# Optimization experiments

Hardware: AMD Instinct MI355X
Metric: run time of the kernel (lower is better)

## Reference

```python
import jax, jax.numpy as jnp
import numpy as np

NEG_SLOPE = 0.2   # PyG GATConv default negative_slope
NUM_GRAPHS = 64   # graphs per batched timestep (max batch id + 1)


def setup_inputs() -> dict:
    key = jax.random.key(0)
    ks = jax.random.split(key, 16)
    T, N, E, F, H, C, B = 8, 20000, 320000, 128, 128, 16, NUM_GRAPHS
    x = jax.random.normal(ks[0], (T, N, F), dtype=jnp.float32)
    edge_index = jax.random.randint(ks[1], (T, 2, E), 0, N, dtype=jnp.int32)
    batch = jnp.sort(jax.random.randint(ks[2], (N,), 0, B, dtype=jnp.int32))
    z = jax.random.normal(ks[3], (B, H), dtype=jnp.float32)
    s_f = 1.0 / np.sqrt(F)
    s_h = 1.0 / np.sqrt(H)
    return {
        "x": x, "edge_index": edge_index, "batch": batch, "z": z,
        "gat_W": jax.random.normal(ks[4], (F, H), jnp.float32) * s_f,
        "att_src": jax.random.normal(ks[5], (H,), jnp.float32) * s_h,
        "att_dst": jax.random.normal(ks[6], (H,), jnp.float32) * s_h,
        "gat_bias": jnp.zeros((H,), jnp.float32),
        "W_ih": jax.random.normal(ks[7], (4 * H, H), jnp.float32) * s_h,
        "W_hh": jax.random.normal(ks[8], (4 * H, H), jnp.float32) * s_h,
        "b_ih": jnp.zeros((4 * H,), jnp.float32),
        "b_hh": jnp.zeros((4 * H,), jnp.float32),
        "fc_W": jax.random.normal(ks[9], (C, 2 * H), jnp.float32) * (1.0 / np.sqrt(2 * H)),
        "fc_b": jnp.zeros((C,), jnp.float32),
    }


def _gat_conv(x, edge_index, W, a_src, a_dst, bias):
    # PyG GATConv, heads=1, add_self_loops=True: gather -> softmax-per-target -> scatter
    N = x.shape[0]
    h = x @ W                                        # [N, H]
    loops = jnp.arange(N, dtype=edge_index.dtype)
    src = jnp.concatenate([edge_index[0], loops])    # message source j
    dst = jnp.concatenate([edge_index[1], loops])    # message target i
    e = jax.nn.leaky_relu((h @ a_src)[src] + (h @ a_dst)[dst], NEG_SLOPE)  # [E+N]
    m = jax.ops.segment_max(e, dst, num_segments=N)  # stable softmax over incoming edges
    w = jnp.exp(e - m[dst])
    denom = jax.ops.segment_sum(w, dst, num_segments=N)
    alpha = w / denom[dst]
    out = jax.ops.segment_sum(alpha[:, None] * h[src], dst, num_segments=N)
    return out + bias


def reference(x, edge_index, batch, z, gat_W, att_src, att_dst, gat_bias,
              W_ih, W_hh, b_ih, b_hh, fc_W, fc_b):
    B = NUM_GRAPHS
    # per-timestep GAT (vmapped over the window) + global mean pool
    node_feats = jax.vmap(lambda xt, ei: _gat_conv(xt, ei, gat_W, att_src, att_dst, gat_bias))(x, edge_index)  # [T,N,H]
    counts = jnp.maximum(jax.ops.segment_sum(jnp.ones_like(batch, jnp.float32), batch, num_segments=B), 1.0)
    pooled = jax.vmap(lambda f: jax.ops.segment_sum(f, batch, num_segments=B))(node_feats) / counts[None, :, None]  # [T,B,H]

    # LSTM over T (PyTorch gate order i, f, g, o)
    H = gat_W.shape[1]
    h0 = jnp.zeros((B, H), x.dtype)

    def step(carry, xt):
        h, c = carry
        gates = xt @ W_ih.T + b_ih + h @ W_hh.T + b_hh
        i, f, g, o = jnp.split(gates, 4, axis=-1)
        c = jax.nn.sigmoid(f) * c + jax.nn.sigmoid(i) * jnp.tanh(g)
        h = jax.nn.sigmoid(o) * jnp.tanh(c)
        return (h, c), None

    (h_n, _), _ = jax.lax.scan(step, (h0, h0), pooled)
    # dropout is identity at inference
    return jnp.concatenate([h_n, z], axis=1) @ fc_W.T + fc_b  # [B, num_classes]
```

## Files before the change

### kernel.cpp

```cpp
#include <hip/hip_runtime.h>
#include <math.h>

#define TT 8
#define NNODES 20000
#define NEDGES 320000
#define FDIM 128
#define HDIM 128
#define BGR 64
#define NCLS 16
#define NBD 157
#define NBS 313
#define CB 80
#define EC 4000
#define CAPD 2816
#define CAPS 1536

__device__ __forceinline__ float lrelu(float x) { return fmaxf(x, 0.2f * x); }
__device__ __forceinline__ float sigmoidf(float x) { return 1.0f / (1.0f + __expf(-x)); }
__device__ __forceinline__ float tanh_fast(float x) {
  return 1.0f - 2.0f / (__expf(2.0f * x) + 1.0f);
}
__device__ __forceinline__ unsigned short f2bf(float f) {
  unsigned int u = __float_as_uint(f);
  unsigned int r = (u + 0x7fff + ((u >> 16) & 1)) >> 16;
  return (unsigned short)r;
}
__device__ __forceinline__ float bf_lo(unsigned int u) { return __uint_as_float(u << 16); }
__device__ __forceinline__ float bf_hi(unsigned int u) { return __uint_as_float(u & 0xffff0000u); }

__global__ __launch_bounds__(256) void k_prep(
    const float* __restrict__ W, const float* __restrict__ att_s, const float* __restrict__ att_d,
    float* __restrict__ u, float* __restrict__ v) {
  const int tid = threadIdx.x;
  if (tid < 128) {
    float su = 0.f, sv = 0.f;
    const float4* wr = (const float4*)(W + (size_t)tid * 128);
    #pragma unroll 8
    for (int q = 0; q < 32; ++q) {
      float4 w4 = wr[q];
      float4 a4 = *(const float4*)(att_s + q * 4);
      float4 d4 = *(const float4*)(att_d + q * 4);
      su += w4.x * a4.x + w4.y * a4.y + w4.z * a4.z + w4.w * a4.w;
      sv += w4.x * d4.x + w4.y * d4.y + w4.z * d4.z + w4.w * d4.w;
    }
    u[tid] = su; v[tid] = sv;
  }
}

__global__ __launch_bounds__(256) void k_gemv(
    const float* __restrict__ x, const float* __restrict__ u, const float* __restrict__ v,
    float* __restrict__ as_, float* __restrict__ ad_, float* __restrict__ denom,
    unsigned int* __restrict__ xb) {
  const int tid = threadIdx.x;
  const int c4 = tid & 31;
  const int ty = tid >> 5;
  const int lane = tid & 63;
  float4 uu = *(const float4*)(u + c4 * 4);
  float4 vv = *(const float4*)(v + c4 * 4);
  const int base = blockIdx.x * 64;
  #pragma unroll
  for (int it = 0; it < 8; ++it) {
    int r = base + it * 8 + ty;
    float4 xv = *(const float4*)(x + (size_t)r * FDIM + c4 * 4);
    float ps = xv.x * uu.x + xv.y * uu.y + xv.z * uu.z + xv.w * uu.w;
    float pd = xv.x * vv.x + xv.y * vv.y + xv.z * vv.z + xv.w * vv.w;
    float4 px;
    px.x = __shfl_xor(xv.x, 16);
    px.y = __shfl_xor(xv.y, 16);
    px.z = __shfl_xor(xv.z, 16);
    px.w = __shfl_xor(xv.w, 16);
    if (c4 < 16) {
      uint4 pk;
      pk.x = (unsigned int)f2bf(xv.x) | ((unsigned int)f2bf(px.x) << 16);
      pk.y = (unsigned int)f2bf(xv.y) | ((unsigned int)f2bf(px.y) << 16);
      pk.z = (unsigned int)f2bf(xv.z) | ((unsigned int)f2bf(px.z) << 16);
      pk.w = (unsigned int)f2bf(xv.w) | ((unsigned int)f2bf(px.w) << 16);
      *(uint4*)(xb + (size_t)r * 64 + c4 * 4) = pk;
    }
    #pragma unroll
    for (int o = 16; o > 0; o >>= 1) { ps += __shfl_xor(ps, o); pd += __shfl_xor(pd, o); }
    if ((lane & 31) == 0) {
      as_[r] = ps;
      ad_[r] = pd;
      denom[r] = __expf(lrelu(ps + pd));
    }
  }
}

__global__ __launch_bounds__(256) void k_scat(
    const int* __restrict__ ei, int* __restrict__ cnt_d, int* __restrict__ cnt_s,
    unsigned int* __restrict__ part_d, unsigned int* __restrict__ part_s) {
  __shared__ unsigned int buf[EC];
  __shared__ int hd[NBD], hs[NBS];
  __shared__ int bd[NBD], bs[NBS];
  const int tid = threadIdx.x;
  const int chunk = blockIdx.x, t = blockIdx.y;
  for (int i = tid; i < NBS; i += 256) { hs[i] = 0; if (i < NBD) hd[i] = 0; }
  __syncthreads();
  const int* eis = ei + (size_t)t * 2 * NEDGES;
  for (int i = tid; i < EC; i += 256) {
    int e = chunk * EC + i;
    int s = eis[e], d = eis[NEDGES + e];
    buf[i] = ((unsigned int)s << 15) | (unsigned int)d;
    atomicAdd(&hd[d >> 7], 1);
    atomicAdd(&hs[s >> 6], 1);
  }
  __syncthreads();
  for (int i = tid; i < NBS; i += 256) {
    bs[i] = atomicAdd(&cnt_s[t * NBS + i], hs[i]);
    hs[i] = 0;
    if (i < NBD) {
      bd[i] = atomicAdd(&cnt_d[t * NBD + i], hd[i]);
      hd[i] = 0;
    }
  }
  __syncthreads();
  unsigned int* pdt = part_d + (size_t)t * NBD * CAPD;
  unsigned int* pst = part_s + (size_t)t * NBS * CAPS;
  for (int i = tid; i < EC; i += 256) {
    unsigned int rec = buf[i];
    int d = rec & 32767, s = rec >> 15;
    int Bd = d >> 7, Bs = s >> 6;
    int od = bd[Bd] + atomicAdd(&hd[Bd], 1);
    pdt[Bd * CAPD + od] = rec;
    int os = bs[Bs] + atomicAdd(&hs[Bs], 1);
    pst[Bs * CAPS + os] = rec;
  }
}

__global__ __launch_bounds__(256) void k_denomB(
    const unsigned int* __restrict__ part_d, const int* __restrict__ cnt_d,
    const float* __restrict__ as_, const float* __restrict__ ad_,
    const float* __restrict__ dseed, const int* __restrict__ batch,
    float4* __restrict__ aux4, int* __restrict__ starts) {
  __shared__ float hist[128];
  __shared__ float adl[128];
  const int tid = threadIdx.x;
  const int B = blockIdx.x, t = blockIdx.y;
  if (tid < 128) {
    hist[tid] = 0.f;
    int n = B * 128 + tid;
    adl[tid] = (n < NNODES) ? ad_[t * NNODES + n] : 0.f;
  }
  __syncthreads();
  const int cnt = cnt_d[t * NBD + B];
  const unsigned int* pdt = part_d + ((size_t)t * NBD + B) * CAPD;
  const float* asb = as_ + (size_t)t * NNODES;
  int i = tid;
  for (; i + 768 < cnt; i += 1024) {
    unsigned int r0 = pdt[i], r1 = pdt[i + 256], r2 = pdt[i + 512], r3 = pdt[i + 768];
    float v0 = asb[r0 >> 15], v1 = asb[r1 >> 15], v2 = asb[r2 >> 15], v3 = asb[r3 >> 15];
    float w0 = __expf(lrelu(v0 + adl[r0 & 127]));
    float w1 = __expf(lrelu(v1 + adl[r1 & 127]));
    float w2 = __expf(lrelu(v2 + adl[r2 & 127]));
    float w3 = __expf(lrelu(v3 + adl[r3 & 127]));
    atomicAdd(&hist[r0 & 127], w0);
    atomicAdd(&hist[r1 & 127], w1);
    atomicAdd(&hist[r2 & 127], w2);
    atomicAdd(&hist[r3 & 127], w3);
  }
  for (; i < cnt; i += 256) {
    unsigned int rec = pdt[i];
    float w = __expf(lrelu(asb[rec >> 15] + adl[rec & 127]));
    atomicAdd(&hist[rec & 127], w);
  }
  __syncthreads();
  if (tid < 128) {
    int n = B * 128 + tid;
    if (n < NNODES) {
      float den = dseed[t * NNODES + n] + hist[tid];
      int bn = batch[n];
      aux4[t * NNODES + n] = make_float4(adl[tid], 1.0f / den, __int_as_float(bn), 0.f);
      if (t == 0) {
        if (n == 0) { for (int bb = 0; bb <= bn; ++bb) starts[bb] = 0; }
        else { int pb = batch[n - 1]; for (int bb = pb + 1; bb <= bn; ++bb) starts[bb] = n; }
        if (n == NNODES - 1) { for (int bb = bn + 1; bb <= BGR; ++bb) starts[bb] = NNODES; }
      }
    }
  }
}

__global__ __launch_bounds__(256) void k_cpgemm(
    const unsigned int* __restrict__ part_s, const int* __restrict__ cnt_s,
    const float* __restrict__ as_, const float4* __restrict__ aux4,
    const unsigned int* __restrict__ xb, unsigned int* __restrict__ ppart) {
  __shared__ float clT[64 * 64];
  const int tid = threadIdx.x;
  const int lane = tid & 63;
  const int B = blockIdx.x, t = blockIdx.y;
  #pragma unroll
  for (int i = tid; i < 64 * 64; i += 256) clT[i] = 0.f;
  const float* asb = as_ + (size_t)t * NNODES;
  float a0 = asb[min(B * 64 + lane, NNODES - 1)];
  __syncthreads();
  const float4* auxt = aux4 + (size_t)t * NNODES;
  if (tid < 64) {
    int n = B * 64 + tid;
    if (n < NNODES) {
      float4 aa = auxt[n];
      float wself = __expf(lrelu(asb[n] + aa.x)) * aa.y;
      atomicAdd(&clT[tid * 64 + __float_as_int(aa.z)], wself);
    }
  }
  {
    const int cnt = cnt_s[t * NBS + B];
    const unsigned int* pst = part_s + ((size_t)t * NBS + B) * CAPS;
    int i = tid;
    for (; i + 768 < cnt; i += 1024) {
      unsigned int r0 = pst[i], r1 = pst[i + 256], r2 = pst[i + 512], r3 = pst[i + 768];
      float4 x0 = auxt[r0 & 32767], x1 = auxt[r1 & 32767];
      float4 x2 = auxt[r2 & 32767], x3 = auxt[r3 & 32767];
      int s0 = (int)(r0 >> 15) & 63, s1 = (int)(r1 >> 15) & 63;
      int s2 = (int)(r2 >> 15) & 63, s3 = (int)(r3 >> 15) & 63;
      float v0 = __shfl(a0, s0), v1 = __shfl(a0, s1);
      float v2 = __shfl(a0, s2), v3 = __shfl(a0, s3);
      float w0 = __expf(lrelu(v0 + x0.x)) * x0.y;
      float w1 = __expf(lrelu(v1 + x1.x)) * x1.y;
      float w2 = __expf(lrelu(v2 + x2.x)) * x2.y;
      float w3 = __expf(lrelu(v3 + x3.x)) * x3.y;
      atomicAdd(&clT[s0 * 64 + __float_as_int(x0.z)], w0);
      atomicAdd(&clT[s1 * 64 + __float_as_int(x1.z)], w1);
      atomicAdd(&clT[s2 * 64 + __float_as_int(x2.z)], w2);
      atomicAdd(&clT[s3 * 64 + __float_as_int(x3.z)], w3);
    }
    for (; i < cnt; i += 256) {
      unsigned int rec = pst[i];
      int s6 = (int)(rec >> 15) & 63;
      float4 aa = auxt[rec & 32767];
      float v = __shfl(a0, s6);
      float w = __expf(lrelu(v + aa.x)) * aa.y;
      atomicAdd(&clT[s6 * 64 + __float_as_int(aa.z)], w);
    }
  }
  __syncthreads();
  const int bq = tid >> 4;
  const int dq = tid & 15;
  const unsigned int* xrow = xb + (size_t)t * NNODES * 64;
  float acc[4][8] = {};
  #pragma unroll 4
  for (int kk = 0; kk < 64; ++kk) {
    int row = B * 64 + kk;
    row = (row < NNODES) ? row : (NNODES - 1);
    uint4 u4 = *(const uint4*)(xrow + (size_t)row * 64 + dq * 4);
    float xd[8];
    xd[0] = bf_lo(u4.x); xd[4] = bf_hi(u4.x);
    xd[1] = bf_lo(u4.y); xd[5] = bf_hi(u4.y);
    xd[2] = bf_lo(u4.z); xd[6] = bf_hi(u4.z);
    xd[3] = bf_lo(u4.w); xd[7] = bf_hi(u4.w);
    float cv[4];
    *(float4*)cv = *(const float4*)&clT[kk * 64 + bq * 4];
    #pragma unroll
    for (int i = 0; i < 4; ++i)
      #pragma unroll
      for (int d = 0; d < 8; ++d)
        acc[i][d] += cv[i] * xd[d];
  }
  unsigned int* pp = ppart + ((size_t)t * NBS + B) * BGR * 64;
  #pragma unroll
  for (int i = 0; i < 4; ++i) {
    uint4 pk;
    pk.x = (unsigned int)f2bf(acc[i][0]) | ((unsigned int)f2bf(acc[i][4]) << 16);
    pk.y = (unsigned int)f2bf(acc[i][1]) | ((unsigned int)f2bf(acc[i][5]) << 16);
    pk.z = (unsigned int)f2bf(acc[i][2]) | ((unsigned int)f2bf(acc[i][6]) << 16);
    pk.w = (unsigned int)f2bf(acc[i][3]) | ((unsigned int)f2bf(acc[i][7]) << 16);
    *(uint4*)(pp + (bq * 4 + i) * 64 + dq * 4) = pk;
  }
}

__global__ __launch_bounds__(128) void k_pw(
    const unsigned int* __restrict__ ppart, const int* __restrict__ starts,
    const float* __restrict__ W, const float* __restrict__ gat_bias,
    float* __restrict__ pooled) {
  __shared__ float srow[128];
  __shared__ float psum[2][128];
  const int tb = blockIdx.x;
  const int t = tb >> 6, b = tb & 63;
  const int d = threadIdx.x & 63, half = threadIdx.x >> 6;
  {
    float slo = 0.f, shi = 0.f;
    const int B0 = half ? 157 : 0, B1 = half ? NBS : 157;
    const unsigned int* pp = ppart + ((size_t)t * NBS * BGR + b) * 64 + d;
    #pragma unroll 4
    for (int B = B0; B < B1; ++B) {
      unsigned int u = pp[(size_t)B * BGR * 64];
      slo += bf_lo(u); shi += bf_hi(u);
    }
    psum[half][d] = slo; psum[half][64 + d] = shi;
  }
  __syncthreads();
  if (threadIdx.x < 128) srow[threadIdx.x] = psum[0][threadIdx.x] + psum[1][threadIdx.x];
  __syncthreads();
  const float invc = 1.0f / (float)max(starts[b + 1] - starts[b], 1);
  const int dd = threadIdx.x;
  float o = 0.f;
  #pragma unroll 8
  for (int k = 0; k < 128; ++k) o += srow[k] * W[k * 128 + dd];
  pooled[(size_t)(t * BGR + b) * HDIM + dd] = o * invc + gat_bias[dd];
}

__global__ __launch_bounds__(512) void k_lstm_fc(
    const float* __restrict__ pooled,
    const float* __restrict__ W_ih, const float* __restrict__ W_hh,
    const float* __restrict__ b_ih, const float* __restrict__ b_hh,
    const float* __restrict__ z, const float* __restrict__ fc_W,
    const float* __restrict__ fc_b, float* __restrict__ out) {
  const int b = blockIdx.x;
  const int g = threadIdx.x;
  __shared__ unsigned int wpk[512 * 65];
  __shared__ float hv[128], cv[128], part[512];
  __shared__ float pool8[TT][128];
  __shared__ float fcp[16][17];

  #pragma unroll 2
  for (int it = 0; it < 64; ++it) {
    int i = g + it * 512;
    int gr = i >> 6, j = i & 63;
    float2 wv = *(const float2*)(W_hh + (size_t)gr * HDIM + j * 2);
    wpk[gr * 65 + j] = (unsigned int)f2bf(wv.x) | ((unsigned int)f2bf(wv.y) << 16);
  }
  #pragma unroll
  for (int i = 0; i < 2; ++i) {
    int idx = g + i * 512;
    int t = idx >> 7, k = idx & 127;
    pool8[t][k] = pooled[((size_t)t * BGR + b) * HDIM + k];
  }
  if (g < 128) { hv[g] = 0.f; cv[g] = 0.f; }
  __syncthreads();

  float gx[8] = {};
  {
    const float4* wi = (const float4*)(W_ih + (size_t)g * HDIM);
    #pragma unroll 2
    for (int k4 = 0; k4 < 32; ++k4) {
      float4 wv = wi[k4];
      #pragma unroll
      for (int t = 0; t < TT; ++t) {
        float4 p = *(const float4*)(&pool8[t][k4 * 4]);
        gx[t] += wv.x * p.x + wv.y * p.y + wv.z * p.z + wv.w * p.w;
      }
    }
  }
  const float bsum = b_ih[g] + b_hh[g];
  const unsigned int* wr = &wpk[g * 65];
  const float4* hv4 = (const float4*)hv;
  #pragma unroll
  for (int t = 0; t < TT; ++t) {
    float s = gx[t] + bsum;
    #pragma unroll 8
    for (int j2 = 0; j2 < 32; ++j2) {
      unsigned int w0 = wr[2 * j2], w1 = wr[2 * j2 + 1];
      float4 hh = hv4[j2];
      s += bf_lo(w0) * hh.x + bf_hi(w0) * hh.y + bf_lo(w1) * hh.z + bf_hi(w1) * hh.w;
    }
    part[g] = s;
    __syncthreads();
    if (g < 128) {
      float ig = sigmoidf(part[g]);
      float fg = sigmoidf(part[128 + g]);
      float gc = tanh_fast(part[256 + g]);
      float og = sigmoidf(part[384 + g]);
      float c = fg * cv[g] + ig * gc;
      cv[g] = c;
      hv[g] = og * tanh_fast(c);
    }
    __syncthreads();
  }
  if (g < 256) {
    const int c = g >> 4, kp = g & 15;
    float s = 0.f;
    for (int k = kp * 16; k < kp * 16 + 16; ++k) {
      float v = (k < 128) ? hv[k] : z[(size_t)b * HDIM + (k - 128)];
      s += v * fc_W[(size_t)c * 256 + k];
    }
    fcp[c][kp] = s;
  }
  __syncthreads();
  if (g < 16) {
    float r = fc_b[g];
    #pragma unroll
    for (int k = 0; k < 16; ++k) r += fcp[g][k];
    out[(size_t)b * NCLS + g] = r;
  }
}

extern "C" void kernel_launch(void* const* d_in, const int* in_sizes, int n_in,
                              void* d_out, int out_size, void* d_ws, size_t ws_size,
                              hipStream_t stream) {
  const float* x       = (const float*)d_in[0];
  const int*   ei      = (const int*)d_in[1];
  const int*   batch   = (const int*)d_in[2];
  const float* z       = (const float*)d_in[3];
  const float* gat_W   = (const float*)d_in[4];
  const float* att_src = (const float*)d_in[5];
  const float* att_dst = (const float*)d_in[6];
  const float* gat_bias= (const float*)d_in[7];
  const float* W_ih    = (const float*)d_in[8];
  const float* W_hh    = (const float*)d_in[9];
  const float* b_ih    = (const float*)d_in[10];
  const float* b_hh    = (const float*)d_in[11];
  const float* fc_W    = (const float*)d_in[12];
  const float* fc_b    = (const float*)d_in[13];
  float* out = (float*)d_out;

  char* ws = (char*)d_ws;
  size_t off = 0;
  auto alloc = [&](size_t bytes) {
    void* p = (void*)(ws + off);
    off += (bytes + 255) & ~(size_t)255;
    return p;
  };
  float*  as_    = (float*)alloc((size_t)TT * NNODES * 4);
  float*  ad_    = (float*)alloc((size_t)TT * NNODES * 4);
  float*  denom  = (float*)alloc((size_t)TT * NNODES * 4);
  float4* aux4   = (float4*)alloc((size_t)TT * NNODES * 16);
  int*    cnt_d  = (int*)alloc((size_t)TT * NBD * 4);
  int*    cnt_s  = (int*)alloc((size_t)TT * NBS * 4);
  unsigned int* part_d = (unsigned int*)alloc(((size_t)TT * NBD + 1) * CAPD * 4);
  unsigned int* part_s = (unsigned int*)alloc(((size_t)TT * NBS + 1) * CAPS * 4);
  unsigned int* ppart  = (unsigned int*)alloc((size_t)TT * NBS * BGR * 64 * 4);
  unsigned int* xb     = (unsigned int*)alloc((size_t)TT * NNODES * 64 * 4);
  float* uvec  = (float*)alloc(128 * 4);
  float* vvec  = (float*)alloc(128 * 4);
  float* pooled = (float*)alloc((size_t)TT * BGR * HDIM * 4);
  int* starts = (int*)alloc((BGR + 1) * 4);
  (void)ws_size; (void)in_sizes; (void)n_in; (void)out_size;

  hipMemsetAsync(cnt_d, 0, (size_t)TT * NBD * 4, stream);
  hipMemsetAsync(cnt_s, 0, (size_t)TT * NBS * 4, stream);

  k_prep<<<1, 256, 0, stream>>>(gat_W, att_src, att_dst, uvec, vvec);
  k_gemv<<<(TT * NNODES) / 64, 256, 0, stream>>>(x, uvec, vvec, as_, ad_, denom, xb);
  k_scat<<<dim3(CB, TT), 256, 0, stream>>>(ei, cnt_d, cnt_s, part_d, part_s);
  k_denomB<<<dim3(NBD, TT), 256, 0, stream>>>(part_d, cnt_d, as_, ad_, denom, batch, aux4, starts);
  k_cpgemm<<<dim3(NBS, TT), 256, 0, stream>>>(part_s, cnt_s, as_, aux4, xb, ppart);
  k_pw<<<TT * BGR, 128, 0, stream>>>(ppart, starts, gat_W, gat_bias, pooled);
  k_lstm_fc<<<BGR, 512, 0, stream>>>(pooled, W_ih, W_hh, b_ih, b_hh, z, fc_W, fc_b, out);
}
```

Before: 190.6 us.

## Use bf16 MFMA for the per-block coefficient-times-features GEMM in k_cpgemm

Replaces the scalar FMA loop that multiplies the 64x64 per-block attention-coefficient matrix by bf16 node features with MFMA 16x16x32 bf16 instructions. The coefficient matrix is converted to bf16 and the feature tile is transposed into shared memory, reusing the coefficient buffer's LDS region, so MFMA fragments can be loaded as short8 vectors. This aims to cut ALU time in this kernel. In exchange it adds two extra LDS staging passes and barriers, and rounds the coefficients to bf16, which lowers precision.

```diff
diff --git a/kernel.cpp b/kernel.cpp
--- a/kernel.cpp
+++ b/kernel.cpp
@@ -14,6 +14,9 @@
 #define EC 4000
 #define CAPD 2816
 #define CAPS 1536
+
+typedef short short8 __attribute__((ext_vector_type(8)));
+typedef float f32x4 __attribute__((ext_vector_type(4)));
 
 __device__ __forceinline__ float lrelu(float x) { return fmaxf(x, 0.2f * x); }
 __device__ __forceinline__ float sigmoidf(float x) { return 1.0f / (1.0f + __expf(-x)); }
@@ -184,9 +187,13 @@
     const unsigned int* __restrict__ part_s, const int* __restrict__ cnt_s,
     const float* __restrict__ as_, const float4* __restrict__ aux4,
     const unsigned int* __restrict__ xb, unsigned int* __restrict__ ppart) {
-  __shared__ float clT[64 * 64];
+  __shared__ char lds0[128 * 72 * 2];
+  __shared__ unsigned short clA[64 * 72];
+  float* clT = (float*)lds0;
+  unsigned short* xT = (unsigned short*)lds0;
   const int tid = threadIdx.x;
   const int lane = tid & 63;
+  const int w = tid >> 6;
   const int B = blockIdx.x, t = blockIdx.y;
   #pragma unroll
   for (int i = tid; i < 64 * 64; i += 256) clT[i] = 0.f;
@@ -233,38 +240,56 @@
     }
   }
   __syncthreads();
-  const int bq = tid >> 4;
-  const int dq = tid & 15;
-  const unsigned int* xrow = xb + (size_t)t * NNODES * 64;
-  float acc[4][8] = {};
-  #pragma unroll 4
-  for (int kk = 0; kk < 64; ++kk) {
-    int row = B * 64 + kk;
-    row = (row < NNODES) ? row : (NNODES - 1);
-    uint4 u4 = *(const uint4*)(xrow + (size_t)row * 64 + dq * 4);
-    float xd[8];
-    xd[0] = bf_lo(u4.x); xd[4] = bf_hi(u4.x);
-    xd[1] = bf_lo(u4.y); xd[5] = bf_hi(u4.y);
-    xd[2] = bf_lo(u4.z); xd[6] = bf_hi(u4.z);
-    xd[3] = bf_lo(u4.w); xd[7] = bf_hi(u4.w);
-    float cv[4];
-    *(float4*)cv = *(const float4*)&clT[kk * 64 + bq * 4];
-    #pragma unroll
-    for (int i = 0; i < 4; ++i)
-      #pragma unroll
-      for (int d = 0; d < 8; ++d)
-        acc[i][d] += cv[i] * xd[d];
+  {
+    unsigned int* clAu = (unsigned int*)clA;
+    const int b = tid & 63, seg = tid >> 6;
+    #pragma unroll
+    for (int q = 0; q < 8; ++q) {
+      int up = seg * 8 + q;
+      int k = up * 2;
+      unsigned int pk = (unsigned int)f2bf(clT[k * 64 + b]) |
+                        ((unsigned int)f2bf(clT[(k + 1) * 64 + b]) << 16);
+      clAu[b * 36 + up] = pk;
+    }
+  }
+  __syncthreads();
+  {
+    const unsigned int* xrow = xb + (size_t)t * NNODES * 64;
+    unsigned int* xTu = (unsigned int*)xT;
+    const int j = tid & 63, kp = tid >> 6;
+    #pragma unroll
+    for (int p = 0; p < 8; ++p) {
+      int kk = (kp * 8 + p) * 2;
+      int r0 = B * 64 + kk;     r0 = (r0 < NNODES) ? r0 : (NNODES - 1);
+      int r1 = B * 64 + kk + 1; r1 = (r1 < NNODES) ? r1 : (NNODES - 1);
+      unsigned int ua = xrow[(size_t)r0 * 64 + j];
+      unsigned int ub = xrow[(size_t)r1 * 64 + j];
+      xTu[j * 36 + (kk >> 1)]        = (ua & 0xffffu) | (ub << 16);
+      xTu[(j + 64) * 36 + (kk >> 1)] = (ua >> 16) | (ub & 0xffff0000u);
+    }
+  }
+  __syncthreads();
+  const int ln = lane & 15, hi = lane >> 4;
+  const int bs = w * 16;
+  f32x4 acc[8] = {};
+  #pragma unroll
+  for (int kh = 0; kh < 2; ++kh) {
+    short8 a = *(const short8*)&clA[(bs + ln) * 72 + kh * 32 + hi * 8];
+    #pragma unroll
+    for (int ni = 0; ni < 8; ++ni) {
+      short8 bfr = *(const short8*)&xT[(ni * 16 + ln) * 72 + kh * 32 + hi * 8];
+      acc[ni] = __builtin_amdgcn_mfma_f32_16x16x32_bf16(a, bfr, acc[ni], 0, 0, 0);
+    }
   }
   unsigned int* pp = ppart + ((size_t)t * NBS + B) * BGR * 64;
   #pragma unroll
-  for (int i = 0; i < 4; ++i) {
-    uint4 pk;
-    pk.x = (unsigned int)f2bf(acc[i][0]) | ((unsigned int)f2bf(acc[i][4]) << 16);
-    pk.y = (unsigned int)f2bf(acc[i][1]) | ((unsigned int)f2bf(acc[i][5]) << 16);
-    pk.z = (unsigned int)f2bf(acc[i][2]) | ((unsigned int)f2bf(acc[i][6]) << 16);
-    pk.w = (unsigned int)f2bf(acc[i][3]) | ((unsigned int)f2bf(acc[i][7]) << 16);
-    *(uint4*)(pp + (bq * 4 + i) * 64 + dq * 4) = pk;
-  }
+  for (int ni = 0; ni < 4; ++ni)
+    #pragma unroll
+    for (int r = 0; r < 4; ++r) {
+      unsigned int pk = (unsigned int)f2bf(acc[ni][r]) |
+                        ((unsigned int)f2bf(acc[ni + 4][r]) << 16);
+      pp[(bs + hi * 4 + r) * 64 + ni * 16 + ln] = pk;
+    }
 }
 
 __global__ __launch_bounds__(128) void k_pw(
```

After: 168.0 us. -11.9%, faster.
